# Kernel tuning notes

Measured on AMD Instinct MI355X. Metric: run time of the kernel, lower is better.

Reference implementation:

```python
import jax, jax.numpy as jnp
import numpy as np

N, K, E = 20000, 4, 320000
IN_DIM, H_IN, D = 1024, 256, 128
GATE_IN = 2 * D + 1  # [h || m || logdeg]
GATE_H = 128         # max(d_out, 32)
TEMP = 0.6
M_CLAMP = 20.0


def _init(key, shape, fan_in):
    return jax.random.normal(key, shape, dtype=jnp.float32) / np.sqrt(fan_in)


def setup_inputs() -> dict:
    key = jax.random.key(0)
    ks = jax.random.split(key, 24)
    inp = {}
    inp['X'] = jax.random.normal(ks[0], (N, IN_DIM), dtype=jnp.float32)
    inp['rows'] = jax.random.randint(ks[1], (K, E), 0, N, dtype=jnp.int32)
    inp['cols'] = jax.random.randint(ks[2], (K, E), 0, N, dtype=jnp.int32)
    inp['mask'] = jnp.ones((N, K), dtype=jnp.float32)
    inp['logdeg'] = jax.random.uniform(ks[3], (N, K), dtype=jnp.float32) * 3.0
    # lin_in: 3-layer MLP 1024 -> 256 -> 256 -> 128, each + ReLU
    inp['W_in0'] = _init(ks[4], (IN_DIM, H_IN), IN_DIM); inp['b_in0'] = jnp.zeros((H_IN,), jnp.float32)
    inp['W_in1'] = _init(ks[5], (H_IN, H_IN), H_IN);     inp['b_in1'] = jnp.zeros((H_IN,), jnp.float32)
    inp['W_in2'] = _init(ks[6], (H_IN, D), H_IN);        inp['b_in2'] = jnp.zeros((D,), jnp.float32)
    # block 0
    inp['Wmsg0'] = _init(ks[7], (D, D), D)
    inp['Wg1_0'] = _init(ks[8], (GATE_IN, GATE_H), GATE_IN); inp['bg1_0'] = jnp.zeros((GATE_H,), jnp.float32)
    inp['Wg2_0'] = _init(ks[9], (GATE_H, 1), GATE_H);        inp['bg2_0'] = jnp.zeros((1,), jnp.float32)
    # block 1
    inp['Wmsg1'] = _init(ks[10], (D, D), D)
    inp['Wg1_1'] = _init(ks[11], (GATE_IN, GATE_H), GATE_IN); inp['bg1_1'] = jnp.zeros((GATE_H,), jnp.float32)
    inp['Wg2_1'] = _init(ks[12], (GATE_H, 1), GATE_H);        inp['bg2_1'] = jnp.zeros((1,), jnp.float32)
    # head
    inp['Wh1'] = _init(ks[13], (D, D), D); inp['bh1'] = jnp.zeros((D,), jnp.float32)
    inp['Wh2'] = _init(ks[14], (D, 1), D); inp['bh2'] = jnp.zeros((1,), jnp.float32)
    return inp


def reference(X, rows, cols, mask, logdeg,
              W_in0, b_in0, W_in1, b_in1, W_in2, b_in2,
              Wmsg0, Wg1_0, bg1_0, Wg2_0, bg2_0,
              Wmsg1, Wg1_1, bg1_1, Wg2_1, bg2_1,
              Wh1, bh1, Wh2, bh2):
    relu = jax.nn.relu
    # input encoder (eval mode: dropout / featdrop are identity)
    H = relu(relu(relu(X @ W_in0 + b_in0) @ W_in1 + b_in1) @ W_in2 + b_in2)

    def pairnorm(x):
        x = x - x.mean(axis=0, keepdims=True)
        mean_norm = jnp.sqrt(jnp.mean(jnp.sum(x * x, axis=1))) + 1e-6
        return x / mean_norm

    def block(H, Wmsg, Wg1, bg1, Wg2, bg2):
        Z = H @ Wmsg  # [N, D]
        def prop(r, c):  # sparse A_k @ Z with binary adjacency: out[r] += Z[c]
            return jax.ops.segment_sum(Z[c], r, num_segments=N)
        M = jnp.transpose(jax.vmap(prop)(rows, cols), (1, 0, 2))  # [N, K, D]
        M = jnp.clip(M, -M_CLAMP, M_CLAMP)
        H_rep = jnp.broadcast_to(H[:, None, :], (N, K, H.shape[1]))
        gate_in = jnp.concatenate([H_rep, M, logdeg[:, :, None]], axis=2)  # [N, K, 2D+1]
        scores = (relu(gate_in @ Wg1 + bg1) @ Wg2 + bg2)[..., 0]  # [N, K]
        alpha = jax.nn.softmax(scores / TEMP, axis=1)
        alpha = alpha * mask
        alpha = alpha / jnp.maximum(alpha.sum(axis=1, keepdims=True), 1e-12)
        alpha = jnp.maximum(alpha, 1e-8)
        alpha = alpha / jnp.maximum(alpha.sum(axis=1, keepdims=True), 1e-12)
        fused = jnp.einsum('nk,nkd->nd', alpha, M)
        return fused, alpha

    fused0, a0 = block(H, Wmsg0, Wg1_0, bg1_0, Wg2_0, bg2_0)
    H = relu(pairnorm(fused0 + H))
    fused1, a1 = block(H, Wmsg1, Wg1_1, bg1_1, Wg2_1, bg2_1)
    H = relu(pairnorm(fused1 + H))

    h = relu(relu(H) @ Wh1 + bh1)
    logits = (h @ Wh2 + bh2)[:, 0]  # [N]
    return logits, jnp.stack([a0, a1], axis=0)
```

## Files before the change

### kernel.cpp

```cpp
#include <hip/hip_runtime.h>
#include <hip/hip_bf16.h>

#define N_NODES 20000
#define KADJ 4
#define NEDGE 320000
#define ETOTAL (KADJ * NEDGE)
#define IN_DIM_ 1024
#define H_IN_ 256
#define DDIM 128
#define GATE_H_ 128
#define TEMP_ 0.6f
#define M_CLAMP_ 20.0f
#define CSR_TOTAL (KADJ * N_NODES)
#define NCOARSE 128
#define QPER (CSR_TOTAL / NCOARSE)
#define ESTRIDE 12288
#define TILE_A 4096
#define BINA_NB ((ETOTAL + TILE_A - 1) / TILE_A)
#define NB_CAST (N_NODES * IN_DIM_ / 8 / 256)
#define NB_TRANS 2560

typedef __attribute__((ext_vector_type(8))) short frag_ab;
typedef __attribute__((ext_vector_type(4))) float frag_cd;
typedef __attribute__((ext_vector_type(8))) unsigned short us8;

__device__ inline unsigned short f2bf(float f) {
    unsigned int u = __float_as_uint(f);
    u += 0x7FFFu + ((u >> 16) & 1);
    return (unsigned short)(u >> 16);
}
__device__ inline float bflo(unsigned int p) { return __uint_as_float(p << 16); }
__device__ inline float bfhi(unsigned int p) { return __uint_as_float(p & 0xffff0000u); }

__device__ __forceinline__ void gld16(const unsigned short* g, unsigned short* l) {
    __builtin_amdgcn_global_load_lds(
        (const __attribute__((address_space(1))) void*)g,
        (__attribute__((address_space(3))) void*)l, 16, 0, 0);
}

#define PIPE_WAIT_N(n)    asm volatile("s_waitcnt vmcnt(" #n ")" ::: "memory")
#define PIPE_WAIT_LAST()  asm volatile("s_waitcnt vmcnt(0)" ::: "memory")
#define PIPE_BAR()        __builtin_amdgcn_s_barrier()
#define PIPE_FENCE()      __builtin_amdgcn_sched_barrier(0)

struct TD { const float* src; unsigned short* dst; int K; int N; };
struct TD10 { TD d[10]; };

__global__ __launch_bounds__(256) void prep_kernel(
    const float* __restrict__ X, unsigned short* __restrict__ Xb,
    TD10 descs,
    const int* __restrict__ rows, const int* __restrict__ cols,
    int* __restrict__ bcnt, uint2* __restrict__ staging)
{
    __shared__ __align__(16) char sraw[2048 + TILE_A * 8];
    int bid = blockIdx.x;
    int tid = threadIdx.x;

    if (bid >= BINA_NB + NB_TRANS) {
        int i = ((bid - BINA_NB - NB_TRANS) * 256 + tid) * 8;
        float4 a = *(const float4*)(X + i), b = *(const float4*)(X + i + 4);
        us8 o;
        o[0] = f2bf(a.x); o[1] = f2bf(a.y); o[2] = f2bf(a.z); o[3] = f2bf(a.w);
        o[4] = f2bf(b.x); o[5] = f2bf(b.y); o[6] = f2bf(b.z); o[7] = f2bf(b.w);
        *(us8*)(Xb + i) = o;
        return;
    }
    if (bid >= BINA_NB) {
        int b2 = bid - BINA_NB;
        TD t = descs.d[b2 >> 8];
        int rem = b2 & 255;
        int n0 = (rem & 7) * 32, k0 = (rem >> 3) * 32;
        if (n0 >= t.N || k0 >= t.K) return;
        float (*tile)[33] = (float(*)[33])sraw;
        int tx = tid & 31, ty4 = (tid >> 5) * 4;
#pragma unroll
        for (int i = 0; i < 4; i++)
            tile[ty4 + i][tx] = t.src[(size_t)(k0 + ty4 + i) * t.N + n0 + tx];
        __syncthreads();
#pragma unroll
        for (int i = 0; i < 4; i++)
            t.dst[(size_t)(n0 + ty4 + i) * t.K + k0 + tx] = f2bf(tile[tx][ty4 + i]);
        return;
    }
    int* hist  = (int*)sraw;
    int* hscan = hist + NCOARSE;
    int* lcur  = hscan + NCOARSE;
    int* gbase = lcur + NCOARSE;
    uint2* pairs = (uint2*)(sraw + 2048);

    int base = bid * TILE_A;
    int cnt_t = min(TILE_A, ETOTAL - base);

    for (int i = tid; i < NCOARSE; i += 256) hist[i] = 0;
    __syncthreads();

    unsigned int q[16], c[16];
    bool valid[16];
#pragma unroll
    for (int i = 0; i < 16; i++) {
        int loc = i * 256 + tid;
        valid[i] = loc < cnt_t;
        if (valid[i]) {
            int e = base + loc;
            int k = e / NEDGE;
            unsigned int qq = (unsigned int)(k * N_NODES + rows[e]);
            q[i] = qq;
            c[i] = (unsigned int)cols[e];
            atomicAdd(&hist[qq / QPER], 1);
        }
    }
    __syncthreads();
    if (tid < NCOARSE) hscan[tid] = hist[tid];
    __syncthreads();
    for (int d = 1; d < NCOARSE; d <<= 1) {
        int v = (tid >= d && tid < NCOARSE) ? hscan[tid - d] : 0;
        __syncthreads();
        if (tid < NCOARSE) hscan[tid] += v;
        __syncthreads();
    }
    if (tid < NCOARSE) {
        int ex = hscan[tid] - hist[tid];
        hscan[tid] = ex;
        lcur[tid] = ex;
        gbase[tid] = hist[tid] ? (tid * ESTRIDE + atomicAdd(&bcnt[tid], hist[tid])) : 0;
    }
    __syncthreads();
#pragma unroll
    for (int i = 0; i < 16; i++) {
        if (valid[i]) {
            int b = q[i] / QPER;
            int p = atomicAdd(&lcur[b], 1);
            pairs[p] = make_uint2(q[i], c[i]);
        }
    }
    __syncthreads();
    for (int i = tid; i < cnt_t; i += 256) {
        uint2 pr = pairs[i];
        int b = pr.x / QPER;
        staging[gbase[b] + (i - hscan[b])] = pr;
    }
}

__global__ __launch_bounds__(256) void gemm64_binb_kernel(
    const unsigned short* __restrict__ A, const unsigned short* __restrict__ Bt,
    const float* __restrict__ bias, unsigned short* __restrict__ Cb,
    int M, int N, int K, int GEMM_NB,
    const uint2* __restrict__ staging, const int* __restrict__ bcnt,
    int* __restrict__ offs, int* __restrict__ ends, int* __restrict__ edst)
{
    __shared__ __align__(16) char smem[49152];
    int tid = threadIdx.x;
    int bid = blockIdx.x;

    if (bid < GEMM_NB) {
        unsigned short* sA0 = (unsigned short*)smem;
        unsigned short* sB0 = (unsigned short*)(smem + 16384);
        int nTn = N >> 7;
        int tileM = (bid / nTn) * 64, tileN = (bid % nTn) * 128;
        int w = tid >> 6, lane = tid & 63;
        int wr = (w & 1) * 32, wc = (w >> 1) * 64;
        int fm = lane & 15, fq = lane >> 4;
        int crow = lane >> 3;
        int gsw = (lane & 7) ^ crow;

        frag_cd acc[2][4] = {};

        auto stage = [&](int buf, int k0) {
#pragma unroll
            for (int t = 0; t < 2; t++) {
                int chunk = w * 2 + t;
                int row = chunk * 8 + crow;
                int ar = min(tileM + row, M - 1);
                gld16(A + (size_t)ar * K + k0 + gsw * 8, sA0 + buf * 4096 + chunk * 512);
            }
#pragma unroll
            for (int t = 0; t < 4; t++) {
                int chunk = w * 4 + t;
                int row = chunk * 8 + crow;
                gld16(Bt + (size_t)(tileN + row) * K + k0 + gsw * 8, sB0 + buf * 8192 + chunk * 512);
            }
        };

        int nt = K >> 6;
        stage(0, 0);
        for (int t = 0; t < nt; t++) {
            int cur = t & 1;
            if (t + 1 < nt) { stage(cur ^ 1, (t + 1) << 6); PIPE_WAIT_N(6); }
            else            { PIPE_WAIT_LAST(); }
            PIPE_BAR();
            PIPE_FENCE();
#pragma unroll
            for (int s = 0; s < 2; s++) {
                int sw = ((s * 4 + fq) ^ (fm & 7)) * 8;
                frag_ab af[2], bf[4];
#pragma unroll
                for (int i = 0; i < 2; i++)
                    af[i] = *(const frag_ab*)(sA0 + cur * 4096 + (wr + i * 16 + fm) * 64 + sw);
#pragma unroll
                for (int j = 0; j < 4; j++)
                    bf[j] = *(const frag_ab*)(sB0 + cur * 8192 + (wc + j * 16 + fm) * 64 + sw);
#pragma unroll
                for (int i = 0; i < 2; i++)
#pragma unroll
                    for (int j = 0; j < 4; j++)
                        acc[i][j] = __builtin_amdgcn_mfma_f32_16x16x32_bf16(af[i], bf[j], acc[i][j], 0, 0, 0);
            }
            PIPE_FENCE();
            PIPE_BAR();
        }
#pragma unroll
        for (int i = 0; i < 2; i++) {
            int row = tileM + wr + i * 16 + fq * 4;
#pragma unroll
            for (int r = 0; r < 4; r++) {
                if (row + r < M) {
#pragma unroll
                    for (int j = 0; j < 4; j++) {
                        int col = tileN + wc + j * 16 + fm;
                        float v = fmaxf(acc[i][j][r] + bias[col], 0.f);
                        Cb[(size_t)(row + r) * N + col] = f2bf(v);
                    }
                }
            }
        }
        return;
    }
    int* cntS = (int*)smem;
    int* sofs = cntS + QPER;
    int* lcur = sofs + QPER;
    int* psum = lcur + QPER;
    int b = bid - GEMM_NB;
    int q0 = b * QPER, base = b * ESTRIDE;
    int fill = bcnt[b];
    for (int i = tid; i < QPER; i += 256) cntS[i] = 0;
    __syncthreads();
    for (int i = tid; i < fill; i += 256)
        atomicAdd(&cntS[staging[base + i].x - q0], 1);
    __syncthreads();
    const int CH = 3;
    int lo = tid * CH, hi = min(lo + CH, QPER);
    int s = 0;
    for (int i = lo; i < hi; i++) s += cntS[i];
    psum[tid] = s;
    __syncthreads();
    for (int d = 1; d < 256; d <<= 1) {
        int v = (tid >= d) ? psum[tid - d] : 0;
        __syncthreads();
        psum[tid] += v;
        __syncthreads();
    }
    int run = (tid == 0) ? 0 : psum[tid - 1];
    for (int i = lo; i < hi; i++) {
        sofs[i] = run;
        lcur[i] = run;
        run += cntS[i];
    }
    __syncthreads();
    for (int i = tid; i < QPER; i += 256) {
        offs[q0 + i] = base + sofs[i];
        ends[q0 + i] = base + sofs[i] + cntS[i];
    }
    for (int i = tid; i < fill; i += 256) {
        uint2 p = staging[base + i];
        int pos = atomicAdd(&lcur[p.x - q0], 1);
        edst[base + pos] = (int)p.y;
    }
}

__global__ __launch_bounds__(256) void gemm_async_kernel(
    const unsigned short* __restrict__ A, const unsigned short* __restrict__ Bt,
    const float* __restrict__ bias, float* __restrict__ Cf, unsigned short* __restrict__ Cb,
    int M, int N, int K, int do_relu)
{
    __shared__ unsigned short sA[2][32 * 64];
    __shared__ unsigned short sB[2][128 * 64];
    int tid = threadIdx.x;
    int tileM = blockIdx.y * 32, tileN = blockIdx.x * 128;
    int w = tid >> 6, lane = tid & 63;
    int wr = (w & 1) * 16, wc = (w >> 1) * 64;
    int fm = lane & 15, fq = lane >> 4;
    int crow = lane >> 3;
    int gsw = (lane & 7) ^ crow;

    frag_cd acc[4] = {};

    auto stage = [&](int buf, int k0) {
        {
            int row = w * 8 + crow;
            int ar = min(tileM + row, M - 1);
            gld16(A + (size_t)ar * K + k0 + gsw * 8, &sA[buf][w * 512]);
        }
#pragma unroll
        for (int t = 0; t < 4; t++) {
            int chunk = w * 4 + t;
            int row = chunk * 8 + crow;
            gld16(Bt + (size_t)(tileN + row) * K + k0 + gsw * 8, &sB[buf][chunk * 512]);
        }
    };

    int nt = K >> 6;
    stage(0, 0);
    for (int t = 0; t < nt; t++) {
        int cur = t & 1;
        if (t + 1 < nt) { stage(cur ^ 1, (t + 1) << 6); PIPE_WAIT_N(5); }
        else            { PIPE_WAIT_LAST(); }
        PIPE_BAR();
        PIPE_FENCE();
#pragma unroll
        for (int s = 0; s < 2; s++) {
            int sw = ((s * 4 + fq) ^ (fm & 7)) * 8;
            frag_ab af = *(const frag_ab*)&sA[cur][(wr + fm) * 64 + sw];
#pragma unroll
            for (int j = 0; j < 4; j++) {
                frag_ab bf = *(const frag_ab*)&sB[cur][(wc + j * 16 + fm) * 64 + sw];
                acc[j] = __builtin_amdgcn_mfma_f32_16x16x32_bf16(af, bf, acc[j], 0, 0, 0);
            }
        }
        PIPE_FENCE();
        PIPE_BAR();
    }
    int row = tileM + wr + fq * 4;
#pragma unroll
    for (int r = 0; r < 4; r++) {
        if (row + r < M) {
#pragma unroll
            for (int j = 0; j < 4; j++) {
                int col = tileN + wc + j * 16 + fm;
                float v = acc[j][r];
                if (bias) v += bias[col];
                if (do_relu) v = fmaxf(v, 0.f);
                if (Cf) Cf[(size_t)(row + r) * N + col] = v;
                if (Cb) Cb[(size_t)(row + r) * N + col] = f2bf(v);
            }
        }
    }
}

__global__ __launch_bounds__(256) void zg_gemm_kernel(
    const unsigned short* __restrict__ A, const unsigned short* __restrict__ Bt,
    const float* __restrict__ bg1, unsigned short* __restrict__ Zb,
    float* __restrict__ GH, int M)
{
    __shared__ unsigned short sA[2][32 * 64];
    __shared__ unsigned short sB[2][128 * 64];
    int tid = threadIdx.x;
    int tileM = blockIdx.y * 32, tileN = blockIdx.x * 128;
    int w = tid >> 6, lane = tid & 63;
    int wr = (w & 1) * 16, wc = (w >> 1) * 64;
    int fm = lane & 15, fq = lane >> 4;
    int crow = lane >> 3;
    int gsw = (lane & 7) ^ crow;

    frag_cd acc[4] = {};

    auto stage = [&](int buf, int k0) {
        {
            int row = w * 8 + crow;
            int ar = min(tileM + row, M - 1);
            gld16(A + (size_t)ar * DDIM + k0 + gsw * 8, &sA[buf][w * 512]);
        }
#pragma unroll
        for (int t = 0; t < 4; t++) {
            int chunk = w * 4 + t;
            int row = chunk * 8 + crow;
            gld16(Bt + (size_t)(tileN + row) * DDIM + k0 + gsw * 8, &sB[buf][chunk * 512]);
        }
    };

    stage(0, 0);
#pragma unroll
    for (int t = 0; t < 2; t++) {
        int cur = t & 1;
        if (t == 0) { stage(1, 64); PIPE_WAIT_N(5); }
        else        { PIPE_WAIT_LAST(); }
        PIPE_BAR();
        PIPE_FENCE();
#pragma unroll
        for (int s = 0; s < 2; s++) {
            int sw = ((s * 4 + fq) ^ (fm & 7)) * 8;
            frag_ab af = *(const frag_ab*)&sA[cur][(wr + fm) * 64 + sw];
#pragma unroll
            for (int j = 0; j < 4; j++) {
                frag_ab bf = *(const frag_ab*)&sB[cur][(wc + j * 16 + fm) * 64 + sw];
                acc[j] = __builtin_amdgcn_mfma_f32_16x16x32_bf16(af, bf, acc[j], 0, 0, 0);
            }
        }
        PIPE_FENCE();
        PIPE_BAR();
    }
    int isZ = (blockIdx.x == 0);
    int row = tileM + wr + fq * 4;
#pragma unroll
    for (int r = 0; r < 4; r++) {
        if (row + r < M) {
#pragma unroll
            for (int j = 0; j < 4; j++) {
                int col = wc + j * 16 + fm;
                float v = acc[j][r];
                if (isZ) Zb[(size_t)(row + r) * DDIM + col] = f2bf(v);
                else     GH[(size_t)(row + r) * GATE_H_ + col] = v + bg1[col];
            }
        }
    }
}

__global__ __launch_bounds__(256) void head_gemm_kernel(
    const unsigned short* __restrict__ A, const unsigned short* __restrict__ Bt,
    const float* __restrict__ bh1, const float* __restrict__ Wh2,
    const float* __restrict__ bh2, float* __restrict__ logits, int M)
{
    __shared__ unsigned short sA[2][32 * 64];
    __shared__ unsigned short sB[2][128 * 64];
    __shared__ float sred[2][32];
    int tid = threadIdx.x;
    int tileM = blockIdx.x * 32;
    int w = tid >> 6, lane = tid & 63;
    int wr = (w & 1) * 16, wc = (w >> 1) * 64;
    int fm = lane & 15, fq = lane >> 4;
    int crow = lane >> 3;
    int gsw = (lane & 7) ^ crow;

    frag_cd acc[4] = {};

    auto stage = [&](int buf, int k0) {
        {
            int row = w * 8 + crow;
            int ar = min(tileM + row, M - 1);
            gld16(A + (size_t)ar * DDIM + k0 + gsw * 8, &sA[buf][w * 512]);
        }
#pragma unroll
        for (int t = 0; t < 4; t++) {
            int chunk = w * 4 + t;
            int row = chunk * 8 + crow;
            gld16(Bt + (size_t)row * DDIM + k0 + gsw * 8, &sB[buf][chunk * 512]);
        }
    };

    stage(0, 0);
#pragma unroll
    for (int t = 0; t < 2; t++) {
        int cur = t & 1;
        if (t == 0) { stage(1, 64); PIPE_WAIT_N(5); }
        else        { PIPE_WAIT_LAST(); }
        PIPE_BAR();
        PIPE_FENCE();
#pragma unroll
        for (int s = 0; s < 2; s++) {
            int sw = ((s * 4 + fq) ^ (fm & 7)) * 8;
            frag_ab af = *(const frag_ab*)&sA[cur][(wr + fm) * 64 + sw];
#pragma unroll
            for (int j = 0; j < 4; j++) {
                frag_ab bf = *(const frag_ab*)&sB[cur][(wc + j * 16 + fm) * 64 + sw];
                acc[j] = __builtin_amdgcn_mfma_f32_16x16x32_bf16(af, bf, acc[j], 0, 0, 0);
            }
        }
        PIPE_FENCE();
        PIPE_BAR();
    }
    float wv[4], bh[4];
#pragma unroll
    for (int j = 0; j < 4; j++) {
        int c = wc + j * 16 + fm;
        wv[j] = Wh2[c];
        bh[j] = bh1[c];
    }
    float part[4];
#pragma unroll
    for (int r = 0; r < 4; r++) {
        float p = 0.f;
#pragma unroll
        for (int j = 0; j < 4; j++) {
            float v = fmaxf(acc[j][r] + bh[j], 0.f);
            p += v * wv[j];
        }
        part[r] = p;
    }
#pragma unroll
    for (int m = 1; m < 16; m <<= 1)
#pragma unroll
        for (int r = 0; r < 4; r++)
            part[r] += __shfl_xor(part[r], m, 64);
    if (fm == 0) {
#pragma unroll
        for (int r = 0; r < 4; r++)
            sred[w >> 1][wr + fq * 4 + r] = part[r];
    }
    __syncthreads();
    if (tid < 32 && tileM + tid < M)
        logits[tileM + tid] = sred[0][tid] + sred[1][tid] + bh2[0];
}

__global__ __launch_bounds__(256) void gather_kernel(
    const int* __restrict__ offs, const int* __restrict__ ends,
    const int* __restrict__ edst,
    const unsigned short* __restrict__ Zb, unsigned short* __restrict__ Mb)
{
    int bid = blockIdx.x;
    int half = (bid >> 2) & 1;
    int qblk = (bid >> 3) * 4 + (bid & 3);
    int w = threadIdx.x >> 6;
    int lane = threadIdx.x & 63;
    int g = lane >> 3;
    int l = lane & 7;
    int q = qblk * 32 + w * 8 + g;
    int k = q / N_NODES;
    int r = q - k * N_NODES;
    int start = offs[q];
    int end = ends[q];
    const unsigned short* Zh = Zb + half * 64 + l * 8;

    float a0 = 0.f, a1 = 0.f, a2 = 0.f, a3 = 0.f;
    float a4 = 0.f, a5 = 0.f, a6 = 0.f, a7 = 0.f;

#define ACC8(P) {                                  \
        a0 += bflo(P.x); a1 += bfhi(P.x);          \
        a2 += bflo(P.y); a3 += bfhi(P.y);          \
        a4 += bflo(P.z); a5 += bfhi(P.z);          \
        a6 += bflo(P.w); a7 += bfhi(P.w); }

    int i = start;
    for (; i + 4 <= end; i += 4) {
        int c0 = edst[i], c1 = edst[i + 1], c2 = edst[i + 2], c3 = edst[i + 3];
        uint4 p0 = *(const uint4*)(Zh + (size_t)c0 * DDIM);
        uint4 p1 = *(const uint4*)(Zh + (size_t)c1 * DDIM);
        uint4 p2 = *(const uint4*)(Zh + (size_t)c2 * DDIM);
        uint4 p3 = *(const uint4*)(Zh + (size_t)c3 * DDIM);
        ACC8(p0); ACC8(p1); ACC8(p2); ACC8(p3);
    }
    for (; i < end; i++) {
        uint4 p0 = *(const uint4*)(Zh + (size_t)edst[i] * DDIM);
        ACC8(p0);
    }
#undef ACC8

#define CLIP(v) fminf(fmaxf(v, -M_CLAMP_), M_CLAMP_)
    unsigned int w0 = (unsigned int)f2bf(CLIP(a0)) | ((unsigned int)f2bf(CLIP(a1)) << 16);
    unsigned int w1 = (unsigned int)f2bf(CLIP(a2)) | ((unsigned int)f2bf(CLIP(a3)) << 16);
    unsigned int w2 = (unsigned int)f2bf(CLIP(a4)) | ((unsigned int)f2bf(CLIP(a5)) << 16);
    unsigned int w3 = (unsigned int)f2bf(CLIP(a6)) | ((unsigned int)f2bf(CLIP(a7)) << 16);
#undef CLIP
    uint4 o = make_uint4(w0, w1, w2, w3);
    *(uint4*)(Mb + ((size_t)r * KADJ + k) * DDIM + half * 64 + l * 8) = o;
}

__global__ __launch_bounds__(256) void gate_fuse_kernel(
    const unsigned short* __restrict__ Mb, const unsigned short* __restrict__ Bt,
    const float* __restrict__ GH, const float* __restrict__ logdeg,
    const float* __restrict__ wld, const float* __restrict__ Wg2,
    const float* __restrict__ bg2, const float* __restrict__ mask,
    const float* __restrict__ H, float* __restrict__ Y,
    float* __restrict__ alpha_out, float* __restrict__ red)
{
    __shared__ unsigned short sA[2][32 * 64];
    __shared__ unsigned short sB[2][128 * 64];
    __shared__ float sred[2][32];
    __shared__ float sc_al[64];
    __shared__ float sx[256], sy[256], sqs[256];
    int tid = threadIdx.x;
    int tile0 = blockIdx.x * 32;
    int node0 = blockIdx.x * 8;
    int w = tid >> 6, lane = tid & 63;
    int wr = (w & 1) * 16, wc = (w >> 1) * 64;
    int fm = lane & 15, fq = lane >> 4;
    int crow = lane >> 3;
    int gsw = (lane & 7) ^ crow;

    frag_cd acc[4] = {};

    auto stage = [&](int buf, int k0) {
        {
            int row = w * 8 + crow;
            gld16(Mb + (size_t)(tile0 + row) * DDIM + k0 + gsw * 8, &sA[buf][w * 512]);
        }
#pragma unroll
        for (int t = 0; t < 4; t++) {
            int chunk = w * 4 + t;
            int row = chunk * 8 + crow;
            gld16(Bt + (size_t)row * DDIM + k0 + gsw * 8, &sB[buf][chunk * 512]);
        }
    };

    stage(0, 0);
#pragma unroll
    for (int t = 0; t < 2; t++) {
        int cur = t & 1;
        if (t == 0) { stage(1, 64); PIPE_WAIT_N(5); }
        else        { PIPE_WAIT_LAST(); }
        PIPE_BAR();
        PIPE_FENCE();
#pragma unroll
        for (int s = 0; s < 2; s++) {
            int sw = ((s * 4 + fq) ^ (fm & 7)) * 8;
            frag_ab af = *(const frag_ab*)&sA[cur][(wr + fm) * 64 + sw];
#pragma unroll
            for (int j = 0; j < 4; j++) {
                frag_ab bf = *(const frag_ab*)&sB[cur][(wc + j * 16 + fm) * 64 + sw];
                acc[j] = __builtin_amdgcn_mfma_f32_16x16x32_bf16(af, bf, acc[j], 0, 0, 0);
            }
        }
        PIPE_FENCE();
        PIPE_BAR();
    }
    float wg2v[4], wldv[4];
#pragma unroll
    for (int j = 0; j < 4; j++) {
        int c = wc + j * 16 + fm;
        wg2v[j] = Wg2[c];
        wldv[j] = wld[c];
    }
    float part[4];
#pragma unroll
    for (int r = 0; r < 4; r++) {
        int q = tile0 + wr + fq * 4 + r;
        int n = q >> 2;
        float ld = logdeg[q];
        float p = 0.f;
#pragma unroll
        for (int j = 0; j < 4; j++) {
            int c = wc + j * 16 + fm;
            float v = acc[j][r] + GH[(size_t)n * GATE_H_ + c] + ld * wldv[j];
            p += fmaxf(v, 0.f) * wg2v[j];
        }
        part[r] = p;
    }
#pragma unroll
    for (int m = 1; m < 16; m <<= 1)
#pragma unroll
        for (int r = 0; r < 4; r++)
            part[r] += __shfl_xor(part[r], m, 64);
    if (fm == 0) {
#pragma unroll
        for (int r = 0; r < 4; r++)
            sred[w >> 1][wr + fq * 4 + r] = part[r];
    }
    __syncthreads();
    if (tid < 32) sc_al[tid] = sred[0][tid] + sred[1][tid] + bg2[0];
    __syncthreads();
    if (tid < 8) {
        int n = node0 + tid;
        float a[KADJ];
        float mx = -1e30f;
#pragma unroll
        for (int k = 0; k < KADJ; k++) {
            a[k] = sc_al[tid * 4 + k] * (1.0f / TEMP_);
            mx = fmaxf(mx, a[k]);
        }
        float sum = 0.f;
#pragma unroll
        for (int k = 0; k < KADJ; k++) { a[k] = expf(a[k] - mx); sum += a[k]; }
#pragma unroll
        for (int k = 0; k < KADJ; k++) a[k] = (a[k] / sum) * mask[(size_t)n * KADJ + k];
        float s2 = 0.f;
#pragma unroll
        for (int k = 0; k < KADJ; k++) s2 += a[k];
        float inv = 1.f / fmaxf(s2, 1e-12f);
#pragma unroll
        for (int k = 0; k < KADJ; k++) a[k] = fmaxf(a[k] * inv, 1e-8f);
        s2 = 0.f;
#pragma unroll
        for (int k = 0; k < KADJ; k++) s2 += a[k];
        inv = 1.f / fmaxf(s2, 1e-12f);
#pragma unroll
        for (int k = 0; k < KADJ; k++) sc_al[32 + tid * 4 + k] = a[k] * inv;
    }
    __syncthreads();
    if (tid < 32) alpha_out[tile0 + tid] = sc_al[32 + tid];
    float csx = 0.f, csy = 0.f, sq = 0.f;
    int j = tid & 63, dd = j * 2;
#pragma unroll
    for (int it = 0; it < 2; it++) {
        int nl = (tid >> 6) + it * 4;
        int n = node0 + nl;
        const float* alp = &sc_al[32 + nl * 4];
        float2 h = *(const float2*)(H + (size_t)n * DDIM + dd);
        float yx = h.x, yy = h.y;
#pragma unroll
        for (int k = 0; k < KADJ; k++) {
            unsigned int u = *(const unsigned int*)(Mb + ((size_t)n * KADJ + k) * DDIM + dd);
            yx += alp[k] * bflo(u);
            yy += alp[k] * bfhi(u);
        }
        *(float2*)(Y + (size_t)n * DDIM + dd) = make_float2(yx, yy);
        csx += yx; csy += yy;
        sq += yx * yx + yy * yy;
    }
    sx[tid] = csx; sy[tid] = csy; sqs[tid] = sq;
    __syncthreads();
    int st = (blockIdx.x & 7) * 132;
    if (tid < 64) {
        float ax = sx[tid] + sx[tid + 64] + sx[tid + 128] + sx[tid + 192];
        float ay = sy[tid] + sy[tid + 64] + sy[tid + 128] + sy[tid + 192];
        atomicAdd(&red[st + tid * 2], ax);
        atomicAdd(&red[st + tid * 2 + 1], ay);
    }
    for (int s = 128; s > 0; s >>= 1) {
        if (tid < s) sqs[tid] += sqs[tid + s];
        __syncthreads();
    }
    if (tid == 0) atomicAdd(&red[st + 128], sqs[0]);
}

__global__ __launch_bounds__(256) void pairnorm_kernel(
    const float* __restrict__ Y, const float* __restrict__ red,
    float* __restrict__ Hout, unsigned short* __restrict__ Hb, int N)
{
    int tid = threadIdx.x;
    int d = tid & 127;
    float invN = 1.0f / (float)N;
    float s = 0.f, rq = 0.f;
#pragma unroll
    for (int st = 0; st < 8; st++) {
        s += red[st * 132 + d];
        rq += red[st * 132 + 128];
    }
    float mu = s * invN;
    __shared__ float smu2[128];
    if (tid < 128) smu2[tid] = mu * mu;
    __syncthreads();
    for (int t = 64; t > 0; t >>= 1) {
        if (tid < t) smu2[tid] += smu2[tid + t];
        __syncthreads();
    }
    float summu2 = smu2[0];
    float var = rq * invN - summu2;
    float norm = sqrtf(fmaxf(var, 0.f)) + 1e-6f;
    float inv = 1.0f / norm;
    int n = blockIdx.x * 2 + (tid >> 7);
    if (n < N) {
        float v = (Y[(size_t)n * DDIM + d] - mu) * inv;
        v = fmaxf(v, 0.f);
        Hout[(size_t)n * DDIM + d] = v;
        Hb[(size_t)n * DDIM + d] = f2bf(v);
    }
}

extern "C" void kernel_launch(void* const* d_in, const int* in_sizes, int n_in,
                              void* d_out, int out_size, void* d_ws, size_t ws_size,
                              hipStream_t stream)
{
    const float* X      = (const float*)d_in[0];
    const int*   rows   = (const int*)d_in[1];
    const int*   cols   = (const int*)d_in[2];
    const float* mask   = (const float*)d_in[3];
    const float* logdeg = (const float*)d_in[4];
    const float* W_in0  = (const float*)d_in[5];
    const float* b_in0  = (const float*)d_in[6];
    const float* W_in1  = (const float*)d_in[7];
    const float* b_in1  = (const float*)d_in[8];
    const float* W_in2  = (const float*)d_in[9];
    const float* b_in2  = (const float*)d_in[10];
    const float* Wmsg[2] = {(const float*)d_in[11], (const float*)d_in[16]};
    const float* Wg1[2]  = {(const float*)d_in[12], (const float*)d_in[17]};
    const float* bg1[2]  = {(const float*)d_in[13], (const float*)d_in[18]};
    const float* Wg2[2]  = {(const float*)d_in[14], (const float*)d_in[19]};
    const float* bg2[2]  = {(const float*)d_in[15], (const float*)d_in[20]};
    const float* Wh1 = (const float*)d_in[21];
    const float* bh1 = (const float*)d_in[22];
    const float* Wh2 = (const float*)d_in[23];
    const float* bh2 = (const float*)d_in[24];

    float* ws = (float*)d_ws;
    unsigned short* Xb  = (unsigned short*)ws;
    unsigned short* Mb  = (unsigned short*)ws;
    float* Ybuf  = ws + 5120000;
    float* GH    = ws + 7680000;
    unsigned short* H0b = (unsigned short*)(ws + 10240000);
    unsigned short* H1b = (unsigned short*)(ws + 12800000);
    unsigned short* Zb  = (unsigned short*)(ws + 12800000);
    uint2* staging = (uint2*)(ws + 15360000);
    float* H     = ws + 15360000;
    unsigned short* Hb = (unsigned short*)(ws + 17920000);
    int*   bcnt  = (int*)(ws + 19200000);
    float* red   = ws + 19200128;
    int*   offs   = (int*)(ws + 19280000);
    int*   ends   = (int*)(ws + 19360000);
    int*   edst   = (int*)(ws + 19440000);
    unsigned short* w0t  = (unsigned short*)(ws + 21013248);
    unsigned short* w1t  = (unsigned short*)(ws + 21144320);
    unsigned short* w2t  = (unsigned short*)(ws + 21177088);
    unsigned short* wzg[2]  = {(unsigned short*)(ws + 21193472), (unsigned short*)(ws + 21209856)};
    unsigned short* wgmt[2] = {(unsigned short*)(ws + 21226240), (unsigned short*)(ws + 21234432)};
    unsigned short* wh1t = (unsigned short*)(ws + 21242624);
    float* logits = (float*)d_out;
    float* alpha_out = (float*)d_out + N_NODES;

    dim3 blk(256);
    int gM32 = (N_NODES + 31) / 32;
    int gM64 = (N_NODES + 63) / 64;

    (void)hipMemsetAsync(bcnt, 0, (128 + 2 * 8 * 132) * sizeof(float), stream);

    TD10 descs;
    descs.d[0] = {W_in0, w0t, IN_DIM_, H_IN_};
    descs.d[1] = {W_in1, w1t, H_IN_, H_IN_};
    descs.d[2] = {W_in2, w2t, H_IN_, DDIM};
    descs.d[3] = {Wmsg[0], wzg[0], DDIM, DDIM};
    descs.d[4] = {Wg1[0], wzg[0] + DDIM * DDIM, DDIM, GATE_H_};
    descs.d[5] = {Wmsg[1], wzg[1], DDIM, DDIM};
    descs.d[6] = {Wg1[1], wzg[1] + DDIM * DDIM, DDIM, GATE_H_};
    descs.d[7] = {Wg1[0] + DDIM * GATE_H_, wgmt[0], DDIM, GATE_H_};
    descs.d[8] = {Wg1[1] + DDIM * GATE_H_, wgmt[1], DDIM, GATE_H_};
    descs.d[9] = {Wh1, wh1t, DDIM, DDIM};
    prep_kernel<<<BINA_NB + NB_TRANS + NB_CAST, blk, 0, stream>>>(
        X, Xb, descs, rows, cols, bcnt, staging);

    gemm64_binb_kernel<<<2 * gM64 + NCOARSE, blk, 0, stream>>>(
        Xb, w0t, b_in0, H0b, N_NODES, H_IN_, IN_DIM_, 2 * gM64,
        staging, bcnt, offs, ends, edst);

    gemm64_binb_kernel<<<2 * gM64, blk, 0, stream>>>(
        H0b, w1t, b_in1, H1b, N_NODES, H_IN_, H_IN_, 2 * gM64,
        nullptr, nullptr, nullptr, nullptr, nullptr);

    gemm_async_kernel<<<dim3(1, gM32), blk, 0, stream>>>(H1b, w2t, b_in2, H, Hb, N_NODES, DDIM, H_IN_, 1);

    for (int b = 0; b < 2; b++) {
        zg_gemm_kernel<<<dim3(2, gM32), blk, 0, stream>>>(Hb, wzg[b], bg1[b], Zb, GH, N_NODES);
        gather_kernel<<<CSR_TOTAL / 16, blk, 0, stream>>>(offs, ends, edst, Zb, Mb);
        float* alph = alpha_out + (size_t)b * N_NODES * KADJ;
        gate_fuse_kernel<<<CSR_TOTAL / 32, blk, 0, stream>>>(
            Mb, wgmt[b], GH, logdeg, Wg1[b] + 256 * GATE_H_, Wg2[b], bg2[b],
            mask, H, Ybuf, alph, red + b * 8 * 132);
        pairnorm_kernel<<<(N_NODES + 1) / 2, blk, 0, stream>>>(Ybuf, red + b * 8 * 132, H, Hb, N_NODES);
    }

    head_gemm_kernel<<<gM32, blk, 0, stream>>>(Hb, wh1t, bh1, Wh2, bh2, logits, N_NODES);
}
```

Baseline: 399.6 us.

## Fuse fp32-to-bf16 cast of X into first GEMM and unroll gather by 8

Removes the separate cast pass that wrote a bf16 copy of X. The first encoder GEMM now loads fp32 X rows into registers, converts them to bf16 and writes them into LDS, while B is still staged with async global-to-LDS loads. This saves one write and one read of the 20000x1024 activation, but the A-side loads become synchronous register loads that need an extra lgkmcnt wait. It also adds a separate plain GEMM kernel for the second layer and an 8-way unrolled gather loop to raise memory-level parallelism.

```diff
diff --git a/kernel.cpp b/kernel.cpp
--- a/kernel.cpp
+++ b/kernel.cpp
@@ -17,7 +17,6 @@
 #define ESTRIDE 12288
 #define TILE_A 4096
 #define BINA_NB ((ETOTAL + TILE_A - 1) / TILE_A)
-#define NB_CAST (N_NODES * IN_DIM_ / 8 / 256)
 #define NB_TRANS 2560
 
 typedef __attribute__((ext_vector_type(8))) short frag_ab;
@@ -40,6 +39,7 @@
 
 #define PIPE_WAIT_N(n)    asm volatile("s_waitcnt vmcnt(" #n ")" ::: "memory")
 #define PIPE_WAIT_LAST()  asm volatile("s_waitcnt vmcnt(0)" ::: "memory")
+#define PIPE_LGKM0()      asm volatile("s_waitcnt lgkmcnt(0)" ::: "memory")
 #define PIPE_BAR()        __builtin_amdgcn_s_barrier()
 #define PIPE_FENCE()      __builtin_amdgcn_sched_barrier(0)
 
@@ -47,7 +47,6 @@
 struct TD10 { TD d[10]; };
 
 __global__ __launch_bounds__(256) void prep_kernel(
-    const float* __restrict__ X, unsigned short* __restrict__ Xb,
     TD10 descs,
     const int* __restrict__ rows, const int* __restrict__ cols,
     int* __restrict__ bcnt, uint2* __restrict__ staging)
@@ -56,15 +55,6 @@
     int bid = blockIdx.x;
     int tid = threadIdx.x;
 
-    if (bid >= BINA_NB + NB_TRANS) {
-        int i = ((bid - BINA_NB - NB_TRANS) * 256 + tid) * 8;
-        float4 a = *(const float4*)(X + i), b = *(const float4*)(X + i + 4);
-        us8 o;
-        o[0] = f2bf(a.x); o[1] = f2bf(a.y); o[2] = f2bf(a.z); o[3] = f2bf(a.w);
-        o[4] = f2bf(b.x); o[5] = f2bf(b.y); o[6] = f2bf(b.z); o[7] = f2bf(b.w);
-        *(us8*)(Xb + i) = o;
-        return;
-    }
     if (bid >= BINA_NB) {
         int b2 = bid - BINA_NB;
         TD t = descs.d[b2 >> 8];
@@ -141,8 +131,8 @@
     }
 }
 
-__global__ __launch_bounds__(256) void gemm64_binb_kernel(
-    const unsigned short* __restrict__ A, const unsigned short* __restrict__ Bt,
+__global__ __launch_bounds__(256) void gemm1f_binb_kernel(
+    const float* __restrict__ Xf, const unsigned short* __restrict__ Bt,
     const float* __restrict__ bias, unsigned short* __restrict__ Cb,
     int M, int N, int K, int GEMM_NB,
     const uint2* __restrict__ staging, const int* __restrict__ bcnt,
@@ -164,15 +154,20 @@
         int gsw = (lane & 7) ^ crow;
 
         frag_cd acc[2][4] = {};
-
-        auto stage = [&](int buf, int k0) {
+        float4 fa[4];
+
+        auto loadA = [&](int k0) {
 #pragma unroll
             for (int t = 0; t < 2; t++) {
                 int chunk = w * 2 + t;
                 int row = chunk * 8 + crow;
                 int ar = min(tileM + row, M - 1);
-                gld16(A + (size_t)ar * K + k0 + gsw * 8, sA0 + buf * 4096 + chunk * 512);
-            }
+                const float* src = Xf + (size_t)ar * K + k0 + gsw * 8;
+                fa[t * 2]     = *(const float4*)(src);
+                fa[t * 2 + 1] = *(const float4*)(src + 4);
+            }
+        };
+        auto stageB = [&](int buf, int k0) {
 #pragma unroll
             for (int t = 0; t < 4; t++) {
                 int chunk = w * 4 + t;
@@ -180,13 +175,37 @@
                 gld16(Bt + (size_t)(tileN + row) * K + k0 + gsw * 8, sB0 + buf * 8192 + chunk * 512);
             }
         };
+        auto writeA = [&](int buf) {
+#pragma unroll
+            for (int t = 0; t < 2; t++) {
+                int chunk = w * 2 + t;
+                float4 a = fa[t * 2], b2 = fa[t * 2 + 1];
+                us8 o;
+                o[0] = f2bf(a.x);  o[1] = f2bf(a.y);  o[2] = f2bf(a.z);  o[3] = f2bf(a.w);
+                o[4] = f2bf(b2.x); o[5] = f2bf(b2.y); o[6] = f2bf(b2.z); o[7] = f2bf(b2.w);
+                *(us8*)&sA0[buf * 4096 + chunk * 512 + lane * 8] = o;
+            }
+        };
 
         int nt = K >> 6;
-        stage(0, 0);
+        loadA(0);
+        PIPE_FENCE();
+        stageB(0, 0);
+        PIPE_FENCE();
+        writeA(0);
         for (int t = 0; t < nt; t++) {
             int cur = t & 1;
-            if (t + 1 < nt) { stage(cur ^ 1, (t + 1) << 6); PIPE_WAIT_N(6); }
-            else            { PIPE_WAIT_LAST(); }
+            if (t + 1 < nt) {
+                loadA((t + 1) << 6);
+                PIPE_FENCE();
+                stageB(cur ^ 1, (t + 1) << 6);
+                PIPE_FENCE();
+                writeA(cur ^ 1);
+                PIPE_WAIT_N(4);
+            } else {
+                PIPE_WAIT_LAST();
+            }
+            PIPE_LGKM0();
             PIPE_BAR();
             PIPE_FENCE();
 #pragma unroll
@@ -264,6 +283,87 @@
         uint2 p = staging[base + i];
         int pos = atomicAdd(&lcur[p.x - q0], 1);
         edst[base + pos] = (int)p.y;
+    }
+}
+
+__global__ __launch_bounds__(256) void gemm64_kernel(
+    const unsigned short* __restrict__ A, const unsigned short* __restrict__ Bt,
+    const float* __restrict__ bias, unsigned short* __restrict__ Cb,
+    int M, int N, int K)
+{
+    __shared__ __align__(16) char smem[49152];
+    int tid = threadIdx.x;
+    int bid = blockIdx.x;
+
+    unsigned short* sA0 = (unsigned short*)smem;
+    unsigned short* sB0 = (unsigned short*)(smem + 16384);
+    int nTn = N >> 7;
+    int tileM = (bid / nTn) * 64, tileN = (bid % nTn) * 128;
+    int w = tid >> 6, lane = tid & 63;
+    int wr = (w & 1) * 32, wc = (w >> 1) * 64;
+    int fm = lane & 15, fq = lane >> 4;
+    int crow = lane >> 3;
+    int gsw = (lane & 7) ^ crow;
+
+    frag_cd acc[2][4] = {};
+
+    auto stage = [&](int buf, int k0) {
+#pragma unroll
+        for (int t = 0; t < 2; t++) {
+            int chunk = w * 2 + t;
+            int row = chunk * 8 + crow;
+            int ar = min(tileM + row, M - 1);
+            gld16(A + (size_t)ar * K + k0 + gsw * 8, sA0 + buf * 4096 + chunk * 512);
+        }
+#pragma unroll
+        for (int t = 0; t < 4; t++) {
+            int chunk = w * 4 + t;
+            int row = chunk * 8 + crow;
+            gld16(Bt + (size_t)(tileN + row) * K + k0 + gsw * 8, sB0 + buf * 8192 + chunk * 512);
+        }
+    };
+
+    int nt = K >> 6;
+    stage(0, 0);
+    for (int t = 0; t < nt; t++) {
+        int cur = t & 1;
+        if (t + 1 < nt) { stage(cur ^ 1, (t + 1) << 6); PIPE_WAIT_N(6); }
+        else            { PIPE_WAIT_LAST(); }
+        PIPE_BAR();
+        PIPE_FENCE();
+#pragma unroll
+        for (int s = 0; s < 2; s++) {
+            int sw = ((s * 4 + fq) ^ (fm & 7)) * 8;
+            frag_ab af[2], bf[4];
+#pragma unroll
+            for (int i = 0; i < 2; i++)
+                af[i] = *(const frag_ab*)(sA0 + cur * 4096 + (wr + i * 16 + fm) * 64 + sw);
+#pragma unroll
+            for (int j = 0; j < 4; j++)
+                bf[j] = *(const frag_ab*)(sB0 + cur * 8192 + (wc + j * 16 + fm) * 64 + sw);
+#pragma unroll
+            for (int i = 0; i < 2; i++)
+#pragma unroll
+                for (int j = 0; j < 4; j++)
+                    acc[i][j] = __builtin_amdgcn_mfma_f32_16x16x32_bf16(af[i], bf[j], acc[i][j], 0, 0, 0);
+        }
+        PIPE_FENCE();
+        PIPE_BAR();
+    }
+#pragma unroll
+    for (int i = 0; i < 2; i++) {
+        int row = tileM + wr + i * 16 + fq * 4;
+#pragma unroll
+        for (int r = 0; r < 4; r++) {
+            if (row + r < M) {
+#pragma unroll
+                for (int j = 0; j < 4; j++) {
+                    int col = tileN + wc + j * 16 + fm;
+                    float v = fmaxf(acc[i][j][r] + bias[col], 0.f);
+                    Cb[(size_t)(row + r) * N + col] = f2bf(v);
+                }
+            }
+        }
     }
 }
 
@@ -519,6 +619,20 @@
         a6 += bflo(P.w); a7 += bfhi(P.w); }
 
     int i = start;
+    for (; i + 8 <= end; i += 8) {
+        int c0 = edst[i],     c1 = edst[i + 1], c2 = edst[i + 2], c3 = edst[i + 3];
+        int c4 = edst[i + 4], c5 = edst[i + 5], c6 = edst[i + 6], c7 = edst[i + 7];
+        uint4 p0 = *(const uint4*)(Zh + (size_t)c0 * DDIM);
+        uint4 p1 = *(const uint4*)(Zh + (size_t)c1 * DDIM);
+        uint4 p2 = *(const uint4*)(Zh + (size_t)c2 * DDIM);
+        uint4 p3 = *(const uint4*)(Zh + (size_t)c3 * DDIM);
+        uint4 p4 = *(const uint4*)(Zh + (size_t)c4 * DDIM);
+        uint4 p5 = *(const uint4*)(Zh + (size_t)c5 * DDIM);
+        uint4 p6 = *(const uint4*)(Zh + (size_t)c6 * DDIM);
+        uint4 p7 = *(const uint4*)(Zh + (size_t)c7 * DDIM);
+        ACC8(p0); ACC8(p1); ACC8(p2); ACC8(p3);
+        ACC8(p4); ACC8(p5); ACC8(p6); ACC8(p7);
+    }
     for (; i + 4 <= end; i += 4) {
         int c0 = edst[i], c1 = edst[i + 1], c2 = edst[i + 2], c3 = edst[i + 3];
         uint4 p0 = *(const uint4*)(Zh + (size_t)c0 * DDIM);
@@ -760,7 +874,6 @@
     const float* bh2 = (const float*)d_in[24];
 
     float* ws = (float*)d_ws;
-    unsigned short* Xb  = (unsigned short*)ws;
     unsigned short* Mb  = (unsigned short*)ws;
     float* Ybuf  = ws + 5120000;
     float* GH    = ws + 7680000;
@@ -801,16 +914,15 @@
     descs.d[7] = {Wg1[0] + DDIM * GATE_H_, wgmt[0], DDIM, GATE_H_};
     descs.d[8] = {Wg1[1] + DDIM * GATE_H_, wgmt[1], DDIM, GATE_H_};
     descs.d[9] = {Wh1, wh1t, DDIM, DDIM};
-    prep_kernel<<<BINA_NB + NB_TRANS + NB_CAST, blk, 0, stream>>>(
-        X, Xb, descs, rows, cols, bcnt, staging);
-
-    gemm64_binb_kernel<<<2 * gM64 + NCOARSE, blk, 0, stream>>>(
-        Xb, w0t, b_in0, H0b, N_NODES, H_IN_, IN_DIM_, 2 * gM64,
+    prep_kernel<<<BINA_NB + NB_TRANS, blk, 0, stream>>>(
+        descs, rows, cols, bcnt, staging);
+
+    gemm1f_binb_kernel<<<2 * gM64 + NCOARSE, blk, 0, stream>>>(
+        X, w0t, b_in0, H0b, N_NODES, H_IN_, IN_DIM_, 2 * gM64,
         staging, bcnt, offs, ends, edst);
 
-    gemm64_binb_kernel<<<2 * gM64, blk, 0, stream>>>(
-        H0b, w1t, b_in1, H1b, N_NODES, H_IN_, H_IN_, 2 * gM64,
-        nullptr, nullptr, nullptr, nullptr, nullptr);
+    gemm64_kernel<<<2 * gM64, blk, 0, stream>>>(
+        H0b, w1t, b_in1, H1b, N_NODES, H_IN_, H_IN_);
 
     gemm_async_kernel<<<dim3(1, gM32), blk, 0, stream>>>(H1b, w2t, b_in2, H, Hb, N_NODES, DDIM, H_IN_, 1);
 
```

Measured after the change: 402.0 us. No clear change (+0.6%).
